# Optimization experiments

Measured on AMD Instinct MI355X. Metric: run time of the kernel, lower is better.

Reference implementation:

```python
import jax, jax.numpy as jnp
import numpy as np

B, H, P, D, NF = 16, 16, 128, 128, 12  # patches == head_dim required by lin_qk


def setup_inputs() -> dict:
    key = jax.random.key(0)
    ks = jax.random.split(key, 8)
    return {
        "q": jax.random.normal(ks[0], (B, H, P, D), jnp.float32),
        "k": jax.random.normal(ks[1], (B, H, P, D), jnp.float32),
        "scale": jnp.ones((1,), jnp.float32),  # unused by the original forward
        "grid": jnp.arange(NF, dtype=jnp.float32) + 1.0,
        "base_weight": jax.random.uniform(ks[2], (D, D), jnp.float32),
        "coef_q": jax.random.uniform(ks[3], (D, NF), jnp.float32),
        "coef_k": jax.random.uniform(ks[4], (D, NF), jnp.float32),
        "scale_base": jnp.ones((1, H, P, D), jnp.float32),
        "scale_sp": jnp.ones((1, H, P, D), jnp.float32),
        "w_qk": jax.random.normal(ks[5], (D, D), jnp.float32) / np.float32(np.sqrt(D)),
        "b_qk": jnp.zeros((D,), jnp.float32),
    }


def _branch(x, coef, grid, base_weight, scale_sp, scale_base):
    # base path: SiLU(x) @ W^T  (F.linear semantics)
    base = jax.nn.silu(x) @ base_weight.T
    # KAN sin basis: sin(grid_f * x_d) -> (B,H,P,NF,D); contract coef[d,f]
    s = jnp.sin(grid[:, None] * x[..., None, :])
    f = jnp.einsum('df,bhpfd->bhpd', coef, s)
    return jax.nn.sigmoid(f * scale_sp + base * scale_base)


def reference(q, k, scale, grid, base_weight, coef_q, coef_k, scale_base, scale_sp, w_qk, b_qk):
    # Per-channel sigmoids, then sum over D. The original builds the full
    # (B,H,P,P,D) broadcast tensor sig_q[...,p,None,:] + sig_k[...,None,p',:]
    # and sums over D; that is exactly separable:
    #   sum_d(sig_q[p,d]) + sum_d(sig_k[p',d])
    sq = _branch(q, coef_q, grid, base_weight, scale_sp, scale_base).sum(-1)  # (B,H,P)
    sk = _branch(k, coef_k, grid, base_weight, scale_sp, scale_base).sum(-1)  # (B,H,P)
    f_out = sq[..., :, None] + sk[..., None, :]  # (B,H,P,P)
    f_out = f_out @ w_qk.T + b_qk  # lin_qk: valid because patches == head_dim
    return jax.nn.softmax(f_out, axis=-1)
```

## Files before the change

kernel.cpp:

```cpp
#include <hip/hip_runtime.h>
#include <hip/hip_bf16.h>


typedef float          f32x4 __attribute__((ext_vector_type(4)));
typedef float          f32x2 __attribute__((ext_vector_type(2)));
typedef short          s16x8 __attribute__((ext_vector_type(8)));
typedef int            s32x4 __attribute__((ext_vector_type(4)));
typedef unsigned int   u32x4 __attribute__((ext_vector_type(4)));

#define LOG2E   1.44269504f
#define NLOG2E -1.44269504f
#define INV2PI  0.15915494309189535f

static __device__ __forceinline__ float hw_exp2(float x) {
    float r;
    asm("v_exp_f32 %0, %1" : "=v"(r) : "v"(x));
    return r;
}
static __device__ __forceinline__ float hw_fract(float x) {
    float r;
    asm("v_fract_f32 %0, %1" : "=v"(r) : "v"(x));
    return r;
}
static __device__ __forceinline__ float hw_sin01(float f) {
    float r;
    asm("v_sin_f32 %0, %1" : "=v"(r) : "v"(f));
    return r;
}
static __device__ __forceinline__ float hw_cos01(float f) {
    float r;
    asm("v_cos_f32 %0, %1" : "=v"(r) : "v"(f));
    return r;
}
static __device__ __forceinline__ float fastrcp(float x) {
    return __builtin_amdgcn_rcpf(x);
}
static __device__ __forceinline__ unsigned int cvt_pk_bf16(float lo, float hi) {
    unsigned int r;
    asm("v_cvt_pk_bf16_f32 %0, %1, %2" : "=v"(r) : "v"(lo), "v"(hi));
    return r;
}
static __device__ __forceinline__ float sigmoid_fast(float z) {
    return fastrcp(1.f + hw_exp2(z * NLOG2E));
}
static __device__ __forceinline__ f32x2 pk_mul(f32x2 a, f32x2 b) {
    f32x2 d;
    asm("v_pk_mul_f32 %0, %1, %2" : "=v"(d) : "v"(a), "v"(b));
    return d;
}
static __device__ __forceinline__ f32x2 pk_fma(f32x2 a, f32x2 b, f32x2 c) {
    f32x2 d;
    asm("v_pk_fma_f32 %0, %1, %2, %3" : "=v"(d) : "v"(a), "v"(b), "v"(c));
    return d;
}
static __device__ __forceinline__ f32x2 pk_fma_nc(f32x2 a, f32x2 b, f32x2 c) {
    f32x2 d;
    asm("v_pk_fma_f32 %0, %1, %2, %3 neg_lo:[0,0,1] neg_hi:[0,0,1]"
        : "=v"(d) : "v"(a), "v"(b), "v"(c));
    return d;
}
static __device__ __forceinline__ int swz(int local) {
    return local ^ (((local >> 8) & 7) << 4);
}

__global__ __launch_bounds__(512, 4) void k_branch(
    const float* __restrict__ q, const float* __restrict__ k,
    const float* __restrict__ bw,
    const float* __restrict__ gridv,
    const float* __restrict__ coef_q, const float* __restrict__ coef_k,
    const float* __restrict__ sbase,
    const float* __restrict__ ssp,
    float* __restrict__ sums_lo, float* __restrict__ sums_hi)
{
    __shared__ char smem[32768 + 6144];
    float* cfl = (float*)(smem + 32768);

    const int t = threadIdx.x;
    const int lane = t & 63, w = t >> 6;
    const int wr = w >> 1;
    const int ch = w & 1;
    const int r15 = lane & 15, g4 = lane >> 4;
    const int row0 = blockIdx.x * 64;
    const bool is_q = row0 < 32768;
    const float* X = is_q ? q : k;
    const float* coef = is_q ? coef_q : coef_k;
    const int xrow0 = is_q ? row0 : row0 - 32768;
    const float g1 = gridv[0];
    const float grev = g1 * INV2PI;

    #pragma unroll
    for (int it = 0; it < 4; ++it) {
        int c = it * 512 + t;
        const float4* wp = (const float4*)&bw[(c >> 4) * 128 + (c & 15) * 8];
        float4 w0 = wp[0], w1 = wp[1];
        u32x4 v = {cvt_pk_bf16(w0.x, w0.y), cvt_pk_bf16(w0.z, w0.w),
                   cvt_pk_bf16(w1.x, w1.y), cvt_pk_bf16(w1.z, w1.w)};
        *(u32x4*)(smem + swz(c * 16)) = v;
    }
    #pragma unroll
    for (int it = 0; it < 3; ++it) {
        int e = it * 512 + t;
        float v = coef[e];
        int d = e / 12, u = e - d * 12;
        cfl[u * 128 + d] = v;
    }
    __syncthreads();

    const int xrow = wr * 16 + r15;
    const float* xrowp = &X[(xrow0 + xrow) * 128];
    const int hp = (row0 + xrow) & 2047;
    const float* ssprow = &ssp[hp * 128];

    f32x4 acc[4];
    #pragma unroll
    for (int n = 0; n < 4; ++n) acc[n] = (f32x4){0.f, 0.f, 0.f, 0.f};
    float fv[16];

    #pragma unroll
    for (int s = 0; s < 4; ++s) {
        const float4* xp = (const float4*)&xrowp[s * 32 + g4 * 8];
        float4 x0 = xp[0], x1 = xp[1];
        float xsv[8] = {x0.x, x0.y, x0.z, x0.w, x1.x, x1.y, x1.z, x1.w};
        float sl[8];
        #pragma unroll
        for (int j = 0; j < 8; ++j) {
            float e = hw_exp2(xsv[j] * NLOG2E);
            sl[j] = xsv[j] * fastrcp(1.f + e);
        }
        s32x4 a4 = {(int)cvt_pk_bf16(sl[0], sl[1]), (int)cvt_pk_bf16(sl[2], sl[3]),
                    (int)cvt_pk_bf16(sl[4], sl[5]), (int)cvt_pk_bf16(sl[6], sl[7])};
        s16x8 af = __builtin_bit_cast(s16x8, a4);

        if ((s >> 1) == ch) {
            const int s2 = s & 1;
            const float4* spp = (const float4*)&ssprow[s * 32 + g4 * 8];
            float4 sp0 = spp[0], sp1 = spp[1];
            float spv[8] = {sp0.x, sp0.y, sp0.z, sp0.w,
                            sp1.x, sp1.y, sp1.z, sp1.w};
            #pragma unroll
            for (int j2 = 0; j2 < 4; ++j2) {
                int d = s * 32 + g4 * 8 + j2 * 2;
                float xa = xsv[j2 * 2], xb = xsv[j2 * 2 + 1];
                float ra = hw_fract(grev * xa), rb = hw_fract(grev * xb);
                float sa = hw_sin01(ra), sb = hw_sin01(rb);
                float ca = hw_cos01(ra), cb = hw_cos01(rb);
                f32x2 t2p = {ca + ca, cb + cb};
                f32x2 scur = {sa, sb};
                f32x2 sprev = scur;
                f32x2 f2 = pk_mul(*(const f32x2*)&cfl[d], scur);
                scur = pk_mul(t2p, scur);
                f2 = pk_fma(*(const f32x2*)&cfl[128 + d], scur, f2);
                #pragma unroll
                for (int u = 2; u < 12; ++u) {
                    f32x2 sn = pk_fma_nc(t2p, scur, sprev);
                    f2 = pk_fma(*(const f32x2*)&cfl[u * 128 + d], sn, f2);
                    sprev = scur; scur = sn;
                }
                f32x2 sp2 = {spv[j2 * 2], spv[j2 * 2 + 1]};
                f32x2 r = pk_mul(f2, sp2);
                fv[s2 * 8 + j2 * 2]     = r[0];
                fv[s2 * 8 + j2 * 2 + 1] = r[1];
            }
        }

        #pragma unroll
        for (int n = 0; n < 4; ++n) {
            s16x8 bfw = *(const s16x8*)(smem + swz((ch * 64 + n * 16 + r15) * 256
                                                   + s * 64 + g4 * 16));
            acc[n] = __builtin_amdgcn_mfma_f32_16x16x32_bf16(bfw, af, acc[n], 0, 0, 0);
        }
    }
    __syncthreads();

    float* myfv = (float*)smem + w * 1024;
    #pragma unroll
    for (int s2 = 0; s2 < 2; ++s2) {
        #pragma unroll
        for (int jb = 0; jb < 2; ++jb) {
            int dloc = s2 * 32 + g4 * 8 + jb * 4;
            f32x4 v = {fv[s2*8 + jb*4 + 0], fv[s2*8 + jb*4 + 1],
                       fv[s2*8 + jb*4 + 2], fv[s2*8 + jb*4 + 3]};
            *(f32x4*)&myfv[r15 * 64 + ((dloc + r15 * 4) & 63)] = v;
        }
    }

    float ps = 0.f;
    #pragma unroll
    for (int n = 0; n < 4; ++n) {
        f32x4 fp = *(f32x4*)&myfv[r15 * 64 + ((n * 16 + g4 * 4 + r15 * 4) & 63)];
        float4 sb = *(const float4*)&sbase[hp * 128 + ch * 64 + n * 16 + g4 * 4];
        float sbv[4] = {sb.x, sb.y, sb.z, sb.w};
        #pragma unroll
        for (int reg = 0; reg < 4; ++reg) {
            float z = fp[reg] + acc[n][reg] * sbv[reg];
            ps += sigmoid_fast(z);
        }
    }
    ps += __shfl_xor(ps, 16, 64);
    ps += __shfl_xor(ps, 32, 64);
    if (g4 == 0) {
        (ch ? sums_hi : sums_lo)[row0 + xrow] = ps;
    }
}

__global__ __launch_bounds__(256) void k_attn(
    const float* __restrict__ sums_lo, const float* __restrict__ sums_hi,
    const float* __restrict__ w_qk, const float* __restrict__ b_qk,
    float* __restrict__ out)
{
    __shared__ float skl[128], Tp[2][128], Rp[2][128], Tl[128], Rl[128];
    const int bh = blockIdx.x;
    const int t = threadIdx.x;

    if (t < 128) {
        int idx = 32768 + bh * 128 + t;
        skl[t] = sums_lo[idx] + sums_hi[idx];
    }
    __syncthreads();
    {
        int j = t & 127, ph = t >> 7;
        const float4* wr = (const float4*)&w_qk[j * 128 + ph * 64];
        const float* sk2 = &skl[ph * 64];
        float a = 0.f, r = 0.f;
        #pragma unroll 8
        for (int p4 = 0; p4 < 16; ++p4) {
            float4 w4 = wr[p4];
            a += w4.x * sk2[p4 * 4 + 0] + w4.y * sk2[p4 * 4 + 1] +
                 w4.z * sk2[p4 * 4 + 2] + w4.w * sk2[p4 * 4 + 3];
            r += w4.x + w4.y + w4.z + w4.w;
        }
        Tp[ph][j] = a;
        Rp[ph][j] = r;
    }
    __syncthreads();
    if (t < 128) {
        Tl[t] = Tp[0][t] + Tp[1][t] + b_qk[t];
        Rl[t] = Rp[0][t] + Rp[1][t];
    }
    __syncthreads();

    const int lane = t & 63, w = t >> 6;
    #pragma unroll 8
    for (int it = 0; it < 32; ++it) {
        int row = bh * 128 + it * 4 + w;
        float sqv = sums_lo[row] + sums_hi[row];
        float2 r2 = *(const float2*)&Rl[lane * 2];
        float2 t2 = *(const float2*)&Tl[lane * 2];
        float l0 = __builtin_fmaf(sqv, r2.x, t2.x);
        float l1 = __builtin_fmaf(sqv, r2.y, t2.y);
        float m = fmaxf(l0, l1);
        #pragma unroll
        for (int s = 32; s >= 1; s >>= 1) m = fmaxf(m, __shfl_xor(m, s, 64));
        float e0 = hw_exp2((l0 - m) * LOG2E);
        float e1 = hw_exp2((l1 - m) * LOG2E);
        float sum = e0 + e1;
        #pragma unroll
        for (int w2 = 32; w2 >= 1; w2 >>= 1) sum += __shfl_xor(sum, w2, 64);
        float inv = fastrcp(sum);
        float2 o2 = {e0 * inv, e1 * inv};
        *(float2*)&out[row * 128 + lane * 2] = o2;
    }
}

extern "C" void kernel_launch(void* const* d_in, const int* in_sizes, int n_in,
                              void* d_out, int out_size, void* d_ws, size_t ws_size,
                              hipStream_t stream) {
    (void)in_sizes; (void)n_in; (void)out_size; (void)ws_size;
    const float* q      = (const float*)d_in[0];
    const float* k      = (const float*)d_in[1];
    const float* gridv  = (const float*)d_in[3];
    const float* bw     = (const float*)d_in[4];
    const float* coef_q = (const float*)d_in[5];
    const float* coef_k = (const float*)d_in[6];
    const float* sbase  = (const float*)d_in[7];
    const float* ssp    = (const float*)d_in[8];
    const float* w_qk   = (const float*)d_in[9];
    const float* b_qk   = (const float*)d_in[10];

    float* out  = (float*)d_out;
    float* ws      = (float*)d_ws;
    float* sums_lo = ws;
    float* sums_hi = ws + 65536;

    k_branch<<<1024, 512, 0, stream>>>(q, k, bw, gridv, coef_q, coef_k,
                                       sbase, ssp, sums_lo, sums_hi);
    k_attn<<<256, 256, 0, stream>>>(sums_lo, sums_hi, w_qk, b_qk, out);
}
```

Baseline: 38.36 us.

## Compute sin features in MFMA output layout, drop LDS transpose and barrier

The sin-basis work is reassigned so each lane computes the features for exactly the channels it later holds in the MFMA accumulator. Each lane reloads those x and scale_sp values from global memory, which removes the shared-memory shuffle and the second __syncthreads. The bf16 packing switches from inline v_cvt_pk_bf16 asm to per-element __float2bfloat16, which may cost more instructions. The attention kernel also hoists the Rl/Tl LDS reads out of the row loop.

Result: slower. 42.13 us (+9.8%).

```diff
diff --git a/kernel.cpp b/kernel.cpp
--- a/kernel.cpp
+++ b/kernel.cpp
@@ -5,8 +5,7 @@
 typedef float          f32x4 __attribute__((ext_vector_type(4)));
 typedef float          f32x2 __attribute__((ext_vector_type(2)));
 typedef short          s16x8 __attribute__((ext_vector_type(8)));
-typedef int            s32x4 __attribute__((ext_vector_type(4)));
-typedef unsigned int   u32x4 __attribute__((ext_vector_type(4)));
+typedef unsigned short u16x8 __attribute__((ext_vector_type(8)));
 
 #define LOG2E   1.44269504f
 #define NLOG2E -1.44269504f
@@ -35,9 +34,10 @@
 static __device__ __forceinline__ float fastrcp(float x) {
     return __builtin_amdgcn_rcpf(x);
 }
-static __device__ __forceinline__ unsigned int cvt_pk_bf16(float lo, float hi) {
-    unsigned int r;
-    asm("v_cvt_pk_bf16_f32 %0, %1, %2" : "=v"(r) : "v"(lo), "v"(hi));
+static __device__ __forceinline__ unsigned short f2bf(float f) {
+    __hip_bfloat16 h = __float2bfloat16(f);
+    unsigned short r;
+    __builtin_memcpy(&r, &h, 2);
     return r;
 }
 static __device__ __forceinline__ float sigmoid_fast(float z) {
@@ -93,9 +93,11 @@
         int c = it * 512 + t;
         const float4* wp = (const float4*)&bw[(c >> 4) * 128 + (c & 15) * 8];
         float4 w0 = wp[0], w1 = wp[1];
-        u32x4 v = {cvt_pk_bf16(w0.x, w0.y), cvt_pk_bf16(w0.z, w0.w),
-                   cvt_pk_bf16(w1.x, w1.y), cvt_pk_bf16(w1.z, w1.w)};
-        *(u32x4*)(smem + swz(c * 16)) = v;
+        float wv[8] = {w0.x, w0.y, w0.z, w0.w, w1.x, w1.y, w1.z, w1.w};
+        u16x8 v;
+        #pragma unroll
+        for (int j = 0; j < 8; ++j) v[j] = f2bf(wv[j]);
+        *(u16x8*)(smem + swz(c * 16)) = v;
     }
     #pragma unroll
     for (int it = 0; it < 3; ++it) {
@@ -109,38 +111,35 @@
     const int xrow = wr * 16 + r15;
     const float* xrowp = &X[(xrow0 + xrow) * 128];
     const int hp = (row0 + xrow) & 2047;
-    const float* ssprow = &ssp[hp * 128];
 
     f32x4 acc[4];
     #pragma unroll
     for (int n = 0; n < 4; ++n) acc[n] = (f32x4){0.f, 0.f, 0.f, 0.f};
-    float fv[16];
+    f32x4 fvv[4];
 
     #pragma unroll
     for (int s = 0; s < 4; ++s) {
         const float4* xp = (const float4*)&xrowp[s * 32 + g4 * 8];
         float4 x0 = xp[0], x1 = xp[1];
         float xsv[8] = {x0.x, x0.y, x0.z, x0.w, x1.x, x1.y, x1.z, x1.w};
-        float sl[8];
+        s16x8 af;
         #pragma unroll
         for (int j = 0; j < 8; ++j) {
             float e = hw_exp2(xsv[j] * NLOG2E);
-            sl[j] = xsv[j] * fastrcp(1.f + e);
-        }
-        s32x4 a4 = {(int)cvt_pk_bf16(sl[0], sl[1]), (int)cvt_pk_bf16(sl[2], sl[3]),
-                    (int)cvt_pk_bf16(sl[4], sl[5]), (int)cvt_pk_bf16(sl[6], sl[7])};
-        s16x8 af = __builtin_bit_cast(s16x8, a4);
-
-        if ((s >> 1) == ch) {
-            const int s2 = s & 1;
-            const float4* spp = (const float4*)&ssprow[s * 32 + g4 * 8];
-            float4 sp0 = spp[0], sp1 = spp[1];
-            float spv[8] = {sp0.x, sp0.y, sp0.z, sp0.w,
-                            sp1.x, sp1.y, sp1.z, sp1.w};
+            float s1 = xsv[j] * fastrcp(1.f + e);
+            af[j] = (short)f2bf(s1);
+        }
+
+        {
+            const int dbase = ch * 64 + s * 16 + g4 * 4;
+            float4 xq = *(const float4*)&xrowp[dbase];
+            float4 sq = *(const float4*)&ssp[hp * 128 + dbase];
+            float xqa[4] = {xq.x, xq.y, xq.z, xq.w};
+            float sqa[4] = {sq.x, sq.y, sq.z, sq.w};
             #pragma unroll
-            for (int j2 = 0; j2 < 4; ++j2) {
-                int d = s * 32 + g4 * 8 + j2 * 2;
-                float xa = xsv[j2 * 2], xb = xsv[j2 * 2 + 1];
+            for (int j2 = 0; j2 < 2; ++j2) {
+                int d = dbase + j2 * 2;
+                float xa = xqa[j2 * 2], xb = xqa[j2 * 2 + 1];
                 float ra = hw_fract(grev * xa), rb = hw_fract(grev * xb);
                 float sa = hw_sin01(ra), sb = hw_sin01(rb);
                 float ca = hw_cos01(ra), cb = hw_cos01(rb);
@@ -156,10 +155,10 @@
                     f2 = pk_fma(*(const f32x2*)&cfl[u * 128 + d], sn, f2);
                     sprev = scur; scur = sn;
                 }
-                f32x2 sp2 = {spv[j2 * 2], spv[j2 * 2 + 1]};
+                f32x2 sp2 = {sqa[j2 * 2], sqa[j2 * 2 + 1]};
                 f32x2 r = pk_mul(f2, sp2);
-                fv[s2 * 8 + j2 * 2]     = r[0];
-                fv[s2 * 8 + j2 * 2 + 1] = r[1];
+                fvv[s][j2 * 2]     = r[0];
+                fvv[s][j2 * 2 + 1] = r[1];
             }
         }
 
@@ -170,29 +169,15 @@
             acc[n] = __builtin_amdgcn_mfma_f32_16x16x32_bf16(bfw, af, acc[n], 0, 0, 0);
         }
     }
-    __syncthreads();
-
-    float* myfv = (float*)smem + w * 1024;
-    #pragma unroll
-    for (int s2 = 0; s2 < 2; ++s2) {
-        #pragma unroll
-        for (int jb = 0; jb < 2; ++jb) {
-            int dloc = s2 * 32 + g4 * 8 + jb * 4;
-            f32x4 v = {fv[s2*8 + jb*4 + 0], fv[s2*8 + jb*4 + 1],
-                       fv[s2*8 + jb*4 + 2], fv[s2*8 + jb*4 + 3]};
-            *(f32x4*)&myfv[r15 * 64 + ((dloc + r15 * 4) & 63)] = v;
-        }
-    }
 
     float ps = 0.f;
     #pragma unroll
     for (int n = 0; n < 4; ++n) {
-        f32x4 fp = *(f32x4*)&myfv[r15 * 64 + ((n * 16 + g4 * 4 + r15 * 4) & 63)];
         float4 sb = *(const float4*)&sbase[hp * 128 + ch * 64 + n * 16 + g4 * 4];
         float sbv[4] = {sb.x, sb.y, sb.z, sb.w};
         #pragma unroll
         for (int reg = 0; reg < 4; ++reg) {
-            float z = fp[reg] + acc[n][reg] * sbv[reg];
+            float z = fvv[n][reg] + acc[n][reg] * sbv[reg];
             ps += sigmoid_fast(z);
         }
     }
@@ -240,14 +225,14 @@
     __syncthreads();
 
     const int lane = t & 63, w = t >> 6;
+    const float2 r2 = *(const float2*)&Rl[lane * 2];
+    const float2 t2v = *(const float2*)&Tl[lane * 2];
     #pragma unroll 8
     for (int it = 0; it < 32; ++it) {
         int row = bh * 128 + it * 4 + w;
         float sqv = sums_lo[row] + sums_hi[row];
-        float2 r2 = *(const float2*)&Rl[lane * 2];
-        float2 t2 = *(const float2*)&Tl[lane * 2];
-        float l0 = __builtin_fmaf(sqv, r2.x, t2.x);
-        float l1 = __builtin_fmaf(sqv, r2.y, t2.y);
+        float l0 = __builtin_fmaf(sqv, r2.x, t2v.x);
+        float l1 = __builtin_fmaf(sqv, r2.y, t2v.y);
         float m = fmaxf(l0, l1);
         #pragma unroll
         for (int s = 32; s >= 1; s >>= 1) m = fmaxf(m, __shfl_xor(m, s, 64));
```
